# Optimization experiments

Hardware: AMD Instinct MI355X
Metric: run time of the kernel (lower is better)

The kernel has to match this reference:

```python
import jax, jax.numpy as jnp
import numpy as np

B, L, DIM, DFF = 4, 2048, 1024, 4096
EPS = 1e-5

def setup_inputs() -> dict:
    key = jax.random.key(0)
    ks = jax.random.split(key, 10)
    s = 0.02
    return {
        "x": jax.random.normal(ks[0], (B, L, DIM), dtype=jnp.float32),
        "ln_g": jnp.ones((DIM,), jnp.float32),
        "ln_b": jnp.zeros((DIM,), jnp.float32),
        "phazor": jax.random.normal(ks[1], (DIM, 2), dtype=jnp.float32),
        "phazor_init": jax.random.normal(ks[2], (DIM, 2), dtype=jnp.float32),
        "w1": jax.random.normal(ks[3], (DIM, DFF), dtype=jnp.float32) * s,
        "b1": jnp.zeros((DFF,), jnp.float32),
        "w2": jax.random.normal(ks[4], (DFF, DIM), dtype=jnp.float32) * s,
        "b2": jnp.zeros((DIM,), jnp.float32),
        "last_conv_re": jax.random.normal(ks[5], (B, DIM), dtype=jnp.float32),
        "last_conv_im": jax.random.normal(ks[6], (B, DIM), dtype=jnp.float32),
    }

def layer_norm(x, g, b):
    mu = jnp.mean(x, axis=-1, keepdims=True)
    var = jnp.var(x, axis=-1, keepdims=True)
    return (x - mu) * jax.lax.rsqrt(var + EPS) * g + b

def spiral_conv(x, phazor, phazor_init, last_re, last_im):
    # x: [B, L, D] float32
    Lx = x.shape[1]
    p = jax.lax.complex(phazor[:, 0], phazor[:, 1])          # [D]
    p_init = jax.lax.complex(phazor_init[:, 0], phazor_init[:, 1])
    pa = jnp.abs(p)
    p = p / pa * jnp.exp(-pa)                                 # normalized decay phazor
    t = jnp.arange(Lx)
    prog = p[None, :] ** t[:, None]                           # [L, D] p^t
    filt = prog * p_init[None, :]                             # [L, D]
    ffilt = jnp.fft.fft(filt, n=2 * Lx, axis=0)               # [2L, D]
    xf = jnp.fft.fft(x.astype(jnp.complex64), n=2 * Lx, axis=1)  # [B, 2L, D]
    conv = jnp.fft.ifft(ffilt[None] * xf, axis=1)[:, :Lx]     # [B, L, D]
    last = jax.lax.complex(last_re, last_im)                  # [B, D] (detached state)
    conv_with_past = conv + last[:, None, :] * prog[None] * p[None, None, :]
    return conv_with_past.real

def reference(x, ln_g, ln_b, phazor, phazor_init, w1, b1, w2, b2, last_conv_re, last_conv_im):
    x_ = x
    h = layer_norm(x, ln_g, ln_b)
    h = spiral_conv(h, phazor, phazor_init, last_conv_re, last_conv_im)
    x = h + x_
    x_ = x
    h = layer_norm(x, ln_g, ln_b)  # same LayerNorm params reused, as in the source
    h = jax.nn.silu(h @ w1 + b1) @ w2 + b2  # FFN, dropout=0 (eval)
    return h + x_

if __name__ == "__main__":
    out = reference(**setup_inputs())
    print(out.shape, out.dtype)
```

## Files before the change

### kernel.cpp

```cpp
#include <hip/hip_runtime.h>
#include <stdint.h>
#include <stddef.h>

#define DIMC 1024
#define LSEQ 2048
#define BSZ  4
#define DFFC 4096
#define NTOK (BSZ*LSEQ)
#define NCHUNK 32
#define CHUNK 64

typedef __bf16 bf16x8 __attribute__((ext_vector_type(8)));
typedef float  f32x4  __attribute__((ext_vector_type(4)));

__device__ __forceinline__ unsigned short f2bf(float f) {
  unsigned int u = __float_as_uint(f);
  u += 0x7fffu + ((u >> 16) & 1u);
  return (unsigned short)(u >> 16);
}

__device__ __forceinline__ void async16(const void* g, void* l) {
  __builtin_amdgcn_global_load_lds(
      (const __attribute__((address_space(1))) unsigned int*)(uintptr_t)g,
      (__attribute__((address_space(3))) unsigned int*)(uintptr_t)l,
      16, 0, 0);
}

__device__ __forceinline__ void bar() {
  asm volatile("" ::: "memory");
  __builtin_amdgcn_s_barrier();
  asm volatile("" ::: "memory");
}
#define LGKM0 do { asm volatile("s_waitcnt lgkmcnt(0)" ::: "memory"); \
                   __builtin_amdgcn_sched_barrier(0); } while (0)
#define VMCNT(n) asm volatile("s_waitcnt vmcnt(" #n ")" ::: "memory")
template <int N> __device__ __forceinline__ void vmwait() {
  if constexpr (N == 0) VMCNT(0);
  else if constexpr (N == 3) VMCNT(3);
  else if constexpr (N == 4) VMCNT(4);
  else if constexpr (N == 6) VMCNT(6);
  else if constexpr (N == 8) VMCNT(8);
}
#define MFMA_BF16 __builtin_amdgcn_mfma_f32_16x16x32_bf16

__global__ __launch_bounds__(256) void prep(const float* __restrict__ w1,
                                            const float* __restrict__ w2,
                                            unsigned short* __restrict__ w1t,
                                            unsigned short* __restrict__ w2t,
                                            const float* __restrict__ x,
                                            float* __restrict__ mu,
                                            float* __restrict__ rstd,
                                            float* __restrict__ tokstat) {
  __shared__ float tile[32][33];
  __shared__ float sh[8];
  const int blk = blockIdx.x;
  if (blk < 8192) {
    const float* w; unsigned short* wt; int K, N, bi;
    if (blk < 4096) { w = w1; wt = w1t; K = DIMC; N = DFFC; bi = blk; }
    else            { w = w2; wt = w2t; K = DFFC; N = DIMC; bi = blk - 4096; }
    const int nbx = N / 32;
    const int n0 = (bi % nbx) * 32, k0 = (bi / nbx) * 32;
    const int tx = threadIdx.x & 31, ty = threadIdx.x >> 5;
    #pragma unroll
    for (int i = 0; i < 32; i += 8)
      tile[ty + i][tx] = w[(size_t)(k0 + ty + i) * N + n0 + tx];
    __syncthreads();
    #pragma unroll
    for (int i = 0; i < 32; i += 8)
      wt[(size_t)(n0 + ty + i) * K + k0 + tx] = f2bf(tile[tx][ty + i]);
  } else {
    const int token = blk - 8192;
    const float4* xp = (const float4*)(x + (size_t)token * DIMC);
    float4 v = xp[threadIdx.x];
    float s  = v.x + v.y + v.z + v.w;
    float s2 = v.x*v.x + v.y*v.y + v.z*v.z + v.w*v.w;
    #pragma unroll
    for (int o = 32; o; o >>= 1) { s += __shfl_down(s, o); s2 += __shfl_down(s2, o); }
    const int lane = threadIdx.x & 63, w = threadIdx.x >> 6;
    if (lane == 0) { sh[w] = s; sh[4 + w] = s2; }
    __syncthreads();
    if (threadIdx.x == 0) {
      float ts  = sh[0] + sh[1] + sh[2] + sh[3];
      float ts2 = sh[4] + sh[5] + sh[6] + sh[7];
      float m = ts * (1.f / DIMC);
      float var = ts2 * (1.f / DIMC) - m * m;
      mu[token] = m;
      rstd[token] = rsqrtf(var + 1e-5f);
      tokstat[2 * token] = 0.f;
      tokstat[2 * token + 1] = 0.f;
    }
  }
}

__device__ __forceinline__ void get_p(const float* __restrict__ phazor, int d,
                                      float& p_re, float& p_im) {
  float pre = phazor[2 * d], pim = phazor[2 * d + 1];
  float a = sqrtf(pre * pre + pim * pim);
  float sc = expf(-a) / a;
  p_re = pre * sc;
  p_im = pim * sc;
}

__global__ __launch_bounds__(256) void scan_phase1(const float* __restrict__ x,
                                                   const float* __restrict__ mu,
                                                   const float* __restrict__ rstd,
                                                   const float* __restrict__ g,
                                                   const float* __restrict__ bb,
                                                   const float* __restrict__ phazor,
                                                   float* __restrict__ Sre,
                                                   float* __restrict__ Sim) {
  const int d = blockIdx.x * 256 + threadIdx.x;
  const int c = blockIdx.y;
  const int b = blockIdx.z;
  float p_re, p_im; get_p(phazor, d, p_re, p_im);
  const float gd = g[d], bd = bb[d];
  const int t0 = c * CHUNK;
  const float* xp  = x + ((size_t)(b * LSEQ + t0)) * DIMC + d;
  const float* mup = mu + b * LSEQ + t0;
  const float* rp  = rstd + b * LSEQ + t0;
  float r_re = 0.f, r_im = 0.f;
  #pragma unroll
  for (int s8 = 0; s8 < CHUNK; s8 += 8) {
    float xv[8];
    #pragma unroll
    for (int k = 0; k < 8; ++k) xv[k] = xp[(size_t)(s8 + k) * DIMC];
    #pragma unroll
    for (int k = 0; k < 8; ++k) {
      float hv = (xv[k] - mup[s8 + k]) * rp[s8 + k] * gd + bd;
      float nr = p_re * r_re - p_im * r_im + hv;
      float ni = p_re * r_im + p_im * r_re;
      r_re = nr; r_im = ni;
    }
  }
  const int bd_i = b * DIMC + d;
  Sre[c * (BSZ * DIMC) + bd_i] = r_re;
  Sim[c * (BSZ * DIMC) + bd_i] = r_im;
}

__global__ __launch_bounds__(256) void scan_phase3(const float* __restrict__ x,
                                                   const float* __restrict__ mu,
                                                   const float* __restrict__ rstd,
                                                   const float* __restrict__ g,
                                                   const float* __restrict__ bb,
                                                   const float* __restrict__ phazor,
                                                   const float* __restrict__ phazor_init,
                                                   const float* __restrict__ last_re,
                                                   const float* __restrict__ last_im,
                                                   const float* __restrict__ Sre,
                                                   const float* __restrict__ Sim,
                                                   float* __restrict__ x2,
                                                   float* __restrict__ tokstat) {
  __shared__ float shs[CHUNK][4], shs2[CHUNK][4];
  const int d = blockIdx.x * 256 + threadIdx.x;
  const int c = blockIdx.y;
  const int b = blockIdx.z;
  const int lane = threadIdx.x & 63, wv = threadIdx.x >> 6;
  float p_re, p_im; get_p(phazor, d, p_re, p_im);
  const float pi_re = phazor_init[2 * d], pi_im = phazor_init[2 * d + 1];
  const float gd = g[d], bd_ = bb[d];
  const int bd_i = b * DIMC + d;
  float br = p_re, bi = p_im;
  #pragma unroll
  for (int i = 0; i < 6; ++i) { float t = br * br - bi * bi; bi = 2.f * br * bi; br = t; }
  float r_re = 0.f, r_im = 0.f;
  for (int j0 = 0; j0 < c; j0 += 8) {
    float sr[8], si[8];
    const int jn = (c - j0 < 8) ? (c - j0) : 8;
    for (int k = 0; k < jn; ++k) {
      sr[k] = Sre[(j0 + k) * (BSZ * DIMC) + bd_i];
      si[k] = Sim[(j0 + k) * (BSZ * DIMC) + bd_i];
    }
    for (int k = 0; k < jn; ++k) {
      float nr = br * r_re - bi * r_im + sr[k];
      float ni = br * r_im + bi * r_re + si[k];
      r_re = nr; r_im = ni;
    }
  }
  float er = 1.f, ei = 0.f;
  {
    float qr = br, qi = bi;
    int e = c;
    while (e) {
      if (e & 1) { float t = er * qr - ei * qi; ei = er * qi + ei * qr; er = t; }
      float t2 = qr * qr - qi * qi; qi = 2.f * qr * qi; qr = t2;
      e >>= 1;
    }
  }
  const float lre = last_re[bd_i], lim = last_im[bd_i];
  float q_re = lre * er - lim * ei;
  float q_im = lre * ei + lim * er;
  const int t0 = c * CHUNK;
  const float* xp  = x + ((size_t)(b * LSEQ + t0)) * DIMC + d;
  const float* mup = mu + b * LSEQ + t0;
  const float* rp  = rstd + b * LSEQ + t0;
  float* op = x2 + ((size_t)(b * LSEQ + t0)) * DIMC + d;
  #pragma unroll
  for (int s8 = 0; s8 < CHUNK; s8 += 8) {
    float xv[8];
    #pragma unroll
    for (int k = 0; k < 8; ++k) xv[k] = xp[(size_t)(s8 + k) * DIMC];
    #pragma unroll
    for (int k = 0; k < 8; ++k) {
      float hv = (xv[k] - mup[s8 + k]) * rp[s8 + k] * gd + bd_;
      float nr = p_re * r_re - p_im * r_im + hv;
      float ni = p_re * r_im + p_im * r_re;
      r_re = nr; r_im = ni;
      float nq = p_re * q_re - p_im * q_im;
      q_im = p_re * q_im + p_im * q_re;
      q_re = nq;
      float opv = pi_re * r_re - pi_im * r_im + q_re + xv[k];
      op[(size_t)(s8 + k) * DIMC] = opv;
      float a1 = opv, a2 = opv * opv;
      #pragma unroll
      for (int o = 32; o; o >>= 1) { a1 += __shfl_xor(a1, o); a2 += __shfl_xor(a2, o); }
      if (lane == 0) { shs[s8 + k][wv] = a1; shs2[s8 + k][wv] = a2; }
    }
  }
  __syncthreads();
  if (threadIdx.x < CHUNK) {
    const int s = threadIdx.x;
    float s1 = shs[s][0] + shs[s][1] + shs[s][2] + shs[s][3];
    float s2 = shs2[s][0] + shs2[s][1] + shs2[s][2] + shs2[s][3];
    const int tok = b * LSEQ + t0 + s;
    atomicAdd(&tokstat[2 * tok], s1);
    atomicAdd(&tokstat[2 * tok + 1], s2);
  }
}

__global__ __launch_bounds__(256) void ln_apply(const float* __restrict__ x2,
                                                const float* __restrict__ tokstat,
                                                const float* __restrict__ g,
                                                const float* __restrict__ bb,
                                                unsigned short* __restrict__ out) {
  const int token = blockIdx.x;
  const float s1 = tokstat[2 * token], s2 = tokstat[2 * token + 1];
  const float m = s1 * (1.f / DIMC);
  const float var = s2 * (1.f / DIMC) - m * m;
  const float r = rsqrtf(var + 1e-5f);
  float4 v = ((const float4*)(x2 + (size_t)token * DIMC))[threadIdx.x];
  float4 gv = ((const float4*)g)[threadIdx.x];
  float4 bv = ((const float4*)bb)[threadIdx.x];
  ushort4 o;
  o.x = f2bf((v.x - m) * r * gv.x + bv.x);
  o.y = f2bf((v.y - m) * r * gv.y + bv.y);
  o.z = f2bf((v.z - m) * r * gv.z + bv.z);
  o.w = f2bf((v.w - m) * r * gv.w + bv.w);
  ((ushort4*)(out + (size_t)token * DIMC))[threadIdx.x] = o;
}

template<int BN, int EPI>
__global__ __launch_bounds__(512, 2) void gemm8(const unsigned short* __restrict__ A,
                                                const unsigned short* __restrict__ Bt,
                                                const float* __restrict__ bias,
                                                const float* __restrict__ resid,
                                                void* __restrict__ outp,
                                                int M, int N, int K) {
  constexpr int AUS = 256 * 32;
  constexpr int BUS = BN * 32;
  constexpr int BUFUS = 2 * AUS + 2 * BUS;
  constexpr int NI = (BN == 256) ? 4 : 2;
  constexpr int LDSUS = (2 * BUFUS > 65536) ? 2 * BUFUS : 65536;
  __shared__ __align__(16) unsigned short lds[LDSUS];

  const int tid  = threadIdx.x;
  const int lane = tid & 63;
  const int wave = tid >> 6;
  const int wm = (wave & 1) * 128;
  const int wn = (wave >> 1) * (BN / 4);
  const int r15 = lane & 15;
  const int cus = ((lane >> 4) ^ ((r15 >> 1) & 3)) * 8;

  int bid = blockIdx.x;
  const int cpx = gridDim.x >> 3;
  bid = (bid & 7) * cpx + (bid >> 3);
  const int ntn = N / BN;
  const int tm = (bid / ntn) * 256;
  const int tn = (bid % ntn) * BN;
  const int NT = K >> 6;

  f32x4 acc[8][NI];
  #pragma unroll
  for (int i = 0; i < 8; ++i)
    #pragma unroll
    for (int j = 0; j < NI; ++j) acc[i][j] = (f32x4){0.f, 0.f, 0.f, 0.f};

  auto stageA1 = [&](int buf, int kk, int k0, int half) {
    unsigned short* blk = lds + buf * BUFUS + kk * AUS;
    const unsigned short* g = A + (size_t)tm * K + k0 + kk * 32;
    const int s = half * 512 + tid;
    const int row = s >> 2;
    const int cg = (s & 3) ^ ((s >> 3) & 3);
    async16(g + (size_t)row * K + cg * 8, blk + (size_t)s * 8);
  };
  auto stageB1 = [&](int buf, int kk, int k0, int half) {
    unsigned short* blk = lds + buf * BUFUS + 2 * AUS + kk * BUS;
    const unsigned short* g = Bt + (size_t)tn * K + k0 + kk * 32;
    const int s = half * 512 + tid;
    const int row = s >> 2;
    const int cg = (s & 3) ^ ((s >> 3) & 3);
    async16(g + (size_t)row * K + cg * 8, blk + (size_t)s * 8);
  };
  auto stageBb = [&](int buf, int kk, int k0) {
    if constexpr (BN == 256) stageB1(buf, kk, k0, 1);
  };
  auto rdA = [&](int buf, int kk, int mi) -> bf16x8 {
    return *(const bf16x8*)(lds + buf * BUFUS + kk * AUS + (wm + mi * 16 + r15) * 32 + cus);
  };
  auto rdB = [&](int buf, int kk, int ni) -> bf16x8 {
    return *(const bf16x8*)(lds + buf * BUFUS + 2 * AUS + kk * BUS + (wn + ni * 16 + r15) * 32 + cus);
  };

  bf16x8 af[4], bq[NI];
  constexpr int VMS = (BN == 256) ? 8 : 6;
  constexpr int VMP = (BN == 256) ? 4 : 3;

#define PH(buf, kk, mh, BREAD, WAIT, ...)                                       \
  {                                                                             \
    _Pragma("unroll")                                                           \
    for (int q = 0; q < 4; ++q) af[q] = rdA(buf, kk, (mh) * 4 + q);             \
    if (BREAD) {                                                                \
      _Pragma("unroll")                                                         \
      for (int n = 0; n < NI; ++n) bq[n] = rdB(buf, kk, n);                     \
    }                                                                           \
    __VA_ARGS__;                                                                \
    bar(); LGKM0;                                                               \
    __builtin_amdgcn_s_setprio(1);                                              \
    _Pragma("unroll")                                                           \
    for (int q = 0; q < 4; ++q)                                                 \
      _Pragma("unroll")                                                         \
      for (int n = 0; n < NI; ++n)                                              \
        acc[(mh) * 4 + q][n] = MFMA_BF16(af[q], bq[n], acc[(mh) * 4 + q][n], 0, 0, 0); \
    __builtin_amdgcn_s_setprio(0);                                              \
    WAIT;                                                                       \
    bar();                                                                      \
  }

  stageA1(0, 0, 0, 0); stageA1(0, 0, 0, 1); stageB1(0, 0, 0, 0); stageBb(0, 0, 0);
  stageA1(0, 1, 0, 0); stageA1(0, 1, 0, 1); stageB1(0, 1, 0, 0); stageBb(0, 1, 0);
  stageA1(1, 0, 64, 0); stageA1(1, 0, 64, 1); stageB1(1, 0, 64, 0); stageBb(1, 0, 64);
  vmwait<VMS>();
  bar();

  for (int i = 0; i < NT / 2 - 1; ++i) {
    const int kb = (2 * i + 1) * 64, kc = kb + 64, kd = kc + 64;
    PH(0, 0, 0, 1, ((void)0),    stageA1(1, 1, kb, 0); stageA1(1, 1, kb, 1))
    PH(0, 0, 1, 0, vmwait<VMS>(), stageB1(1, 1, kb, 0); stageBb(1, 1, kb))
    PH(0, 1, 0, 1, ((void)0),    stageA1(0, 0, kc, 0); stageA1(0, 0, kc, 1))
    PH(0, 1, 1, 0, vmwait<VMS>(), stageB1(0, 0, kc, 0); stageBb(0, 0, kc))
    PH(1, 0, 0, 1, ((void)0),    stageA1(0, 1, kc, 0); stageA1(0, 1, kc, 1))
    PH(1, 0, 1, 0, vmwait<VMS>(), stageB1(0, 1, kc, 0); stageBb(0, 1, kc))
    PH(1, 1, 0, 1, ((void)0),    stageA1(1, 0, kd, 0); stageA1(1, 0, kd, 1))
    PH(1, 1, 1, 0, vmwait<VMS>(), stageB1(1, 0, kd, 0); stageBb(1, 0, kd))
  }

  {
    const int kb = (NT - 1) * 64;
    PH(0, 0, 0, 1, ((void)0),    stageA1(1, 1, kb, 0); stageA1(1, 1, kb, 1))
    PH(0, 0, 1, 0, vmwait<VMS>(), stageB1(1, 1, kb, 0); stageBb(1, 1, kb))
    PH(0, 1, 0, 1, ((void)0),    ((void)0))
    PH(0, 1, 1, 0, vmwait<VMP>(), ((void)0))
    PH(1, 0, 0, 1, ((void)0),    ((void)0))
    PH(1, 0, 1, 0, vmwait<0>(),  ((void)0))
    PH(1, 1, 0, 1, ((void)0),    ((void)0))
    PH(1, 1, 1, 0, ((void)0),    ((void)0))
  }
#undef PH

  const int rg = (lane >> 4) * 4;
  float bias_r[NI];
  #pragma unroll
  for (int ni = 0; ni < NI; ++ni) bias_r[ni] = bias[tn + wn + ni * 16 + r15];

  bar();
  if constexpr (EPI == 0) {
    unsigned short* C = lds;
    #pragma unroll
    for (int mi = 0; mi < 8; ++mi)
      #pragma unroll
      for (int ni = 0; ni < NI; ++ni) {
        const int c0 = wn + ni * 16 + r15;
        #pragma unroll
        for (int j = 0; j < 4; ++j) {
          const int r = wm + mi * 16 + rg + j;
          const int key = (((r & 3) ^ ((r >> 2) & 3)) << 4);
          float v = acc[mi][ni][j] + bias_r[ni];
          v = v / (1.f + __expf(-v));
          C[r * 256 + (c0 ^ key)] = f2bf(v);
        }
      }
    bar();
    #pragma unroll
    for (int i = 0; i < 16; ++i) {
      const int off = i * 4096 + tid * 8;
      const int r = off >> 8;
      const int pc = off & 255;
      const int key = (((r & 3) ^ ((r >> 2) & 3)) << 4);
      bf16x8 v = *(const bf16x8*)(C + off);
      *(bf16x8*)((unsigned short*)outp + (size_t)(tm + r) * N + tn + (pc ^ key)) = v;
    }
  } else {
    float* C = (float*)lds;
    #pragma unroll
    for (int mi = 0; mi < 8; ++mi)
      #pragma unroll
      for (int ni = 0; ni < NI; ++ni) {
        const int c0 = wn + ni * 16 + r15;
        #pragma unroll
        for (int j = 0; j < 4; ++j) {
          const int r = wm + mi * 16 + rg + j;
          const int key = (((r & 3) ^ ((r >> 2) & 3)) << 4);
          C[r * 128 + (c0 ^ key)] = acc[mi][ni][j] + bias_r[ni];
        }
      }
    bar();
    #pragma unroll
    for (int i = 0; i < 16; ++i) {
      const int off = i * 2048 + tid * 4;
      const int r = off >> 7;
      const int pc = off & 127;
      const int key = (((r & 3) ^ ((r >> 2) & 3)) << 4);
      f32x4 v = *(const f32x4*)(C + off);
      const size_t gaddr = (size_t)(tm + r) * N + tn + (pc ^ key);
      f32x4 rv = *(const f32x4*)(resid + gaddr);
      v += rv;
      *(f32x4*)((float*)outp + gaddr) = v;
    }
  }
}

extern "C" void kernel_launch(void* const* d_in, const int* in_sizes, int n_in,
                              void* d_out, int out_size, void* d_ws, size_t ws_size,
                              hipStream_t stream) {
  const float* x           = (const float*)d_in[0];
  const float* ln_g        = (const float*)d_in[1];
  const float* ln_b        = (const float*)d_in[2];
  const float* phazor      = (const float*)d_in[3];
  const float* phazor_init = (const float*)d_in[4];
  const float* w1          = (const float*)d_in[5];
  const float* b1          = (const float*)d_in[6];
  const float* w2          = (const float*)d_in[7];
  const float* b2          = (const float*)d_in[8];
  const float* last_re     = (const float*)d_in[9];
  const float* last_im     = (const float*)d_in[10];
  float* out = (float*)d_out;
  char* ws = (char*)d_ws;
  const size_t MB = 1ull << 20;

  float* x2  = (float*)(ws);
  float* mu1 = (float*)(ws + 32 * MB);
  float* rs1 = (float*)(ws + 32 * MB + 64 * 1024);
  float* Sre = (float*)(ws + 32 * MB + 256 * 1024);
  float* Sim = (float*)(ws + 32 * MB + 768 * 1024);
  float* tokstat = (float*)(ws + 32 * MB + 1280 * 1024);
  unsigned short* h2  = (unsigned short*)(ws + 35 * MB);
  unsigned short* hid = (unsigned short*)(ws + 51 * MB);
  unsigned short* w1t = (unsigned short*)(ws + 115 * MB);
  unsigned short* w2t = (unsigned short*)(ws + 123 * MB);

  prep<<<16384, 256, 0, stream>>>(w1, w2, w1t, w2t, x, mu1, rs1, tokstat);
  scan_phase1<<<dim3(DIMC / 256, NCHUNK, BSZ), 256, 0, stream>>>(x, mu1, rs1, ln_g, ln_b,
                                                                 phazor, Sre, Sim);
  scan_phase3<<<dim3(DIMC / 256, NCHUNK, BSZ), 256, 0, stream>>>(x, mu1, rs1, ln_g, ln_b, phazor,
                                                                 phazor_init, last_re, last_im,
                                                                 Sre, Sim, x2, tokstat);
  ln_apply<<<NTOK, 256, 0, stream>>>(x2, tokstat, ln_g, ln_b, h2);

  gemm8<256, 0><<<(NTOK / 256) * (DFFC / 256), 512, 0, stream>>>(h2, w1t, b1, nullptr, hid,
                                                                 NTOK, DFFC, DIMC);
  gemm8<128, 1><<<(NTOK / 256) * (DIMC / 128), 512, 0, stream>>>(hid, w2t, b2, x2, out,
                                                                 NTOK, DIMC, DFFC);
}
```

Before: 349.8 us.

## Replace pipelined 256-row GEMM with simple 128x128 single-buffered GEMM

Replaces the hand-scheduled, double-buffered gemm8 (256xBN tiles, 512 threads, phased barriers with priority hints and async prefetch overlap) with a simpler gemm97 that uses 128x128 tiles and 256 threads. It loads each 64-wide K slice into LDS and syncs before computing, with no overlap of loads and MFMA. The residual epilogue is split into two halves to fit the smaller LDS. This gives more, smaller blocks and lower register and LDS use per block, at the cost of less data reuse per tile and no latency hiding in the K loop.

```diff
diff --git a/kernel.cpp b/kernel.cpp
--- a/kernel.cpp
+++ b/kernel.cpp
@@ -26,21 +26,6 @@
       16, 0, 0);
 }
 
-__device__ __forceinline__ void bar() {
-  asm volatile("" ::: "memory");
-  __builtin_amdgcn_s_barrier();
-  asm volatile("" ::: "memory");
-}
-#define LGKM0 do { asm volatile("s_waitcnt lgkmcnt(0)" ::: "memory"); \
-                   __builtin_amdgcn_sched_barrier(0); } while (0)
-#define VMCNT(n) asm volatile("s_waitcnt vmcnt(" #n ")" ::: "memory")
-template <int N> __device__ __forceinline__ void vmwait() {
-  if constexpr (N == 0) VMCNT(0);
-  else if constexpr (N == 3) VMCNT(3);
-  else if constexpr (N == 4) VMCNT(4);
-  else if constexpr (N == 6) VMCNT(6);
-  else if constexpr (N == 8) VMCNT(8);
-}
 #define MFMA_BF16 __builtin_amdgcn_mfma_f32_16x16x32_bf16
 
 __global__ __launch_bounds__(256) void prep(const float* __restrict__ w1,
@@ -248,136 +233,79 @@
   ((ushort4*)(out + (size_t)token * DIMC))[threadIdx.x] = o;
 }
 
-template<int BN, int EPI>
-__global__ __launch_bounds__(512, 2) void gemm8(const unsigned short* __restrict__ A,
-                                                const unsigned short* __restrict__ Bt,
-                                                const float* __restrict__ bias,
-                                                const float* __restrict__ resid,
-                                                void* __restrict__ outp,
-                                                int M, int N, int K) {
-  constexpr int AUS = 256 * 32;
-  constexpr int BUS = BN * 32;
-  constexpr int BUFUS = 2 * AUS + 2 * BUS;
-  constexpr int NI = (BN == 256) ? 4 : 2;
-  constexpr int LDSUS = (2 * BUFUS > 65536) ? 2 * BUFUS : 65536;
-  __shared__ __align__(16) unsigned short lds[LDSUS];
-
+template<int EPI>
+__global__ __launch_bounds__(256) void gemm97(const unsigned short* __restrict__ A,
+                                              const unsigned short* __restrict__ Bt,
+                                              const float* __restrict__ bias,
+                                              const float* __restrict__ resid,
+                                              void* __restrict__ outp,
+                                              int M, int N, int K) {
+  __shared__ __align__(16) unsigned short As[2 * 128 * 32];
+  __shared__ __align__(16) unsigned short Bs[2 * 128 * 32];
   const int tid  = threadIdx.x;
   const int lane = tid & 63;
   const int wave = tid >> 6;
-  const int wm = (wave & 1) * 128;
-  const int wn = (wave >> 1) * (BN / 4);
+  const int wm = (wave & 1) * 64;
+  const int wn = (wave >> 1) * 64;
   const int r15 = lane & 15;
   const int cus = ((lane >> 4) ^ ((r15 >> 1) & 3)) * 8;
 
   int bid = blockIdx.x;
   const int cpx = gridDim.x >> 3;
   bid = (bid & 7) * cpx + (bid >> 3);
-  const int ntn = N / BN;
-  const int tm = (bid / ntn) * 256;
-  const int tn = (bid % ntn) * BN;
-  const int NT = K >> 6;
-
-  f32x4 acc[8][NI];
+  const int ntn = N >> 7;
+  const int tm = (bid / ntn) << 7;
+  const int tn = (bid % ntn) << 7;
+
+  f32x4 acc[4][4];
   #pragma unroll
-  for (int i = 0; i < 8; ++i)
-    #pragma unroll
-    for (int j = 0; j < NI; ++j) acc[i][j] = (f32x4){0.f, 0.f, 0.f, 0.f};
-
-  auto stageA1 = [&](int buf, int kk, int k0, int half) {
-    unsigned short* blk = lds + buf * BUFUS + kk * AUS;
-    const unsigned short* g = A + (size_t)tm * K + k0 + kk * 32;
-    const int s = half * 512 + tid;
-    const int row = s >> 2;
-    const int cg = (s & 3) ^ ((s >> 3) & 3);
-    async16(g + (size_t)row * K + cg * 8, blk + (size_t)s * 8);
-  };
-  auto stageB1 = [&](int buf, int kk, int k0, int half) {
-    unsigned short* blk = lds + buf * BUFUS + 2 * AUS + kk * BUS;
-    const unsigned short* g = Bt + (size_t)tn * K + k0 + kk * 32;
-    const int s = half * 512 + tid;
-    const int row = s >> 2;
-    const int cg = (s & 3) ^ ((s >> 3) & 3);
-    async16(g + (size_t)row * K + cg * 8, blk + (size_t)s * 8);
-  };
-  auto stageBb = [&](int buf, int kk, int k0) {
-    if constexpr (BN == 256) stageB1(buf, kk, k0, 1);
-  };
-  auto rdA = [&](int buf, int kk, int mi) -> bf16x8 {
-    return *(const bf16x8*)(lds + buf * BUFUS + kk * AUS + (wm + mi * 16 + r15) * 32 + cus);
-  };
-  auto rdB = [&](int buf, int kk, int ni) -> bf16x8 {
-    return *(const bf16x8*)(lds + buf * BUFUS + 2 * AUS + kk * BUS + (wn + ni * 16 + r15) * 32 + cus);
-  };
-
-  bf16x8 af[4], bq[NI];
-  constexpr int VMS = (BN == 256) ? 8 : 6;
-  constexpr int VMP = (BN == 256) ? 4 : 3;
-
-#define PH(buf, kk, mh, BREAD, WAIT, ...)                                       \
-  {                                                                             \
-    _Pragma("unroll")                                                           \
-    for (int q = 0; q < 4; ++q) af[q] = rdA(buf, kk, (mh) * 4 + q);             \
-    if (BREAD) {                                                                \
-      _Pragma("unroll")                                                         \
-      for (int n = 0; n < NI; ++n) bq[n] = rdB(buf, kk, n);                     \
-    }                                                                           \
-    __VA_ARGS__;                                                                \
-    bar(); LGKM0;                                                               \
-    __builtin_amdgcn_s_setprio(1);                                              \
-    _Pragma("unroll")                                                           \
-    for (int q = 0; q < 4; ++q)                                                 \
-      _Pragma("unroll")                                                         \
-      for (int n = 0; n < NI; ++n)                                              \
-        acc[(mh) * 4 + q][n] = MFMA_BF16(af[q], bq[n], acc[(mh) * 4 + q][n], 0, 0, 0); \
-    __builtin_amdgcn_s_setprio(0);                                              \
-    WAIT;                                                                       \
-    bar();                                                                      \
-  }
-
-  stageA1(0, 0, 0, 0); stageA1(0, 0, 0, 1); stageB1(0, 0, 0, 0); stageBb(0, 0, 0);
-  stageA1(0, 1, 0, 0); stageA1(0, 1, 0, 1); stageB1(0, 1, 0, 0); stageBb(0, 1, 0);
-  stageA1(1, 0, 64, 0); stageA1(1, 0, 64, 1); stageB1(1, 0, 64, 0); stageBb(1, 0, 64);
-  vmwait<VMS>();
-  bar();
-
-  for (int i = 0; i < NT / 2 - 1; ++i) {
-    const int kb = (2 * i + 1) * 64, kc = kb + 64, kd = kc + 64;
-    PH(0, 0, 0, 1, ((void)0),    stageA1(1, 1, kb, 0); stageA1(1, 1, kb, 1))
-    PH(0, 0, 1, 0, vmwait<VMS>(), stageB1(1, 1, kb, 0); stageBb(1, 1, kb))
-    PH(0, 1, 0, 1, ((void)0),    stageA1(0, 0, kc, 0); stageA1(0, 0, kc, 1))
-    PH(0, 1, 1, 0, vmwait<VMS>(), stageB1(0, 0, kc, 0); stageBb(0, 0, kc))
-    PH(1, 0, 0, 1, ((void)0),    stageA1(0, 1, kc, 0); stageA1(0, 1, kc, 1))
-    PH(1, 0, 1, 0, vmwait<VMS>(), stageB1(0, 1, kc, 0); stageBb(0, 1, kc))
-    PH(1, 1, 0, 1, ((void)0),    stageA1(1, 0, kd, 0); stageA1(1, 0, kd, 1))
-    PH(1, 1, 1, 0, vmwait<VMS>(), stageB1(1, 0, kd, 0); stageBb(1, 0, kd))
-  }
-
-  {
-    const int kb = (NT - 1) * 64;
-    PH(0, 0, 0, 1, ((void)0),    stageA1(1, 1, kb, 0); stageA1(1, 1, kb, 1))
-    PH(0, 0, 1, 0, vmwait<VMS>(), stageB1(1, 1, kb, 0); stageBb(1, 1, kb))
-    PH(0, 1, 0, 1, ((void)0),    ((void)0))
-    PH(0, 1, 1, 0, vmwait<VMP>(), ((void)0))
-    PH(1, 0, 0, 1, ((void)0),    ((void)0))
-    PH(1, 0, 1, 0, vmwait<0>(),  ((void)0))
-    PH(1, 1, 0, 1, ((void)0),    ((void)0))
-    PH(1, 1, 1, 0, ((void)0),    ((void)0))
-  }
-#undef PH
+  for (int i = 0; i < 4; ++i)
+    #pragma unroll
+    for (int j = 0; j < 4; ++j) acc[i][j] = (f32x4){0.f, 0.f, 0.f, 0.f};
+
+  for (int k0 = 0; k0 < K; k0 += 64) {
+    __syncthreads();
+    #pragma unroll
+    for (int s = 0; s < 4; ++s) {
+      const int slot = s * 256 + tid;
+      const int kk = slot >> 9;
+      const int sl = slot & 511;
+      const int row = sl >> 2;
+      const int cg = (sl & 3) ^ ((row >> 1) & 3);
+      const size_t gcol = k0 + kk * 32 + cg * 8;
+      async16(A  + (size_t)(tm + row) * K + gcol, As + kk * 4096 + (size_t)sl * 8);
+      async16(Bt + (size_t)(tn + row) * K + gcol, Bs + kk * 4096 + (size_t)sl * 8);
+    }
+    __syncthreads();
+    #pragma unroll
+    for (int kk = 0; kk < 2; ++kk) {
+      bf16x8 af[4], bv[4];
+      #pragma unroll
+      for (int mi = 0; mi < 4; ++mi)
+        af[mi] = *(const bf16x8*)(As + kk * 4096 + (wm + mi * 16 + r15) * 32 + cus);
+      #pragma unroll
+      for (int ni = 0; ni < 4; ++ni)
+        bv[ni] = *(const bf16x8*)(Bs + kk * 4096 + (wn + ni * 16 + r15) * 32 + cus);
+      #pragma unroll
+      for (int mi = 0; mi < 4; ++mi)
+        #pragma unroll
+        for (int ni = 0; ni < 4; ++ni)
+          acc[mi][ni] = MFMA_BF16(af[mi], bv[ni], acc[mi][ni], 0, 0, 0);
+    }
+  }
 
   const int rg = (lane >> 4) * 4;
-  float bias_r[NI];
+  float bias_r[4];
   #pragma unroll
-  for (int ni = 0; ni < NI; ++ni) bias_r[ni] = bias[tn + wn + ni * 16 + r15];
-
-  bar();
+  for (int ni = 0; ni < 4; ++ni) bias_r[ni] = bias[tn + wn + ni * 16 + r15];
+
+  __syncthreads();
   if constexpr (EPI == 0) {
-    unsigned short* C = lds;
-    #pragma unroll
-    for (int mi = 0; mi < 8; ++mi)
-      #pragma unroll
-      for (int ni = 0; ni < NI; ++ni) {
+    unsigned short* C = As;
+    #pragma unroll
+    for (int mi = 0; mi < 4; ++mi)
+      #pragma unroll
+      for (int ni = 0; ni < 4; ++ni) {
         const int c0 = wn + ni * 16 + r15;
         #pragma unroll
         for (int j = 0; j < 4; ++j) {
@@ -385,45 +313,51 @@
           const int key = (((r & 3) ^ ((r >> 2) & 3)) << 4);
           float v = acc[mi][ni][j] + bias_r[ni];
           v = v / (1.f + __expf(-v));
-          C[r * 256 + (c0 ^ key)] = f2bf(v);
+          C[r * 128 + (c0 ^ key)] = f2bf(v);
         }
       }
-    bar();
-    #pragma unroll
-    for (int i = 0; i < 16; ++i) {
-      const int off = i * 4096 + tid * 8;
-      const int r = off >> 8;
-      const int pc = off & 255;
+    __syncthreads();
+    #pragma unroll
+    for (int i = 0; i < 8; ++i) {
+      const int off = i * 2048 + tid * 8;
+      const int r = off >> 7;
+      const int pc = off & 127;
       const int key = (((r & 3) ^ ((r >> 2) & 3)) << 4);
       bf16x8 v = *(const bf16x8*)(C + off);
       *(bf16x8*)((unsigned short*)outp + (size_t)(tm + r) * N + tn + (pc ^ key)) = v;
     }
   } else {
-    float* C = (float*)lds;
-    #pragma unroll
-    for (int mi = 0; mi < 8; ++mi)
-      #pragma unroll
-      for (int ni = 0; ni < NI; ++ni) {
-        const int c0 = wn + ni * 16 + r15;
+    float* C = (float*)As;
+    #pragma unroll
+    for (int h = 0; h < 2; ++h) {
+      if (wm == h * 64) {
         #pragma unroll
-        for (int j = 0; j < 4; ++j) {
-          const int r = wm + mi * 16 + rg + j;
-          const int key = (((r & 3) ^ ((r >> 2) & 3)) << 4);
-          C[r * 128 + (c0 ^ key)] = acc[mi][ni][j] + bias_r[ni];
-        }
+        for (int mi = 0; mi < 4; ++mi)
+          #pragma unroll
+          for (int ni = 0; ni < 4; ++ni) {
+            const int c0 = wn + ni * 16 + r15;
+            #pragma unroll
+            for (int j = 0; j < 4; ++j) {
+              const int rl = mi * 16 + rg + j;
+              const int key = (((rl & 3) ^ ((rl >> 2) & 3)) << 4);
+              C[rl * 128 + (c0 ^ key)] = acc[mi][ni][j] + bias_r[ni];
+            }
+          }
       }
-    bar();
-    #pragma unroll
-    for (int i = 0; i < 16; ++i) {
-      const int off = i * 2048 + tid * 4;
-      const int r = off >> 7;
-      const int pc = off & 127;
-      const int key = (((r & 3) ^ ((r >> 2) & 3)) << 4);
-      f32x4 v = *(const f32x4*)(C + off);
-      const size_t gaddr = (size_t)(tm + r) * N + tn + (pc ^ key);
-      f32x4 rv = *(const f32x4*)(resid + gaddr);
-      v += rv;
-      *(f32x4*)((float*)outp + gaddr) = v;
+      __syncthreads();
+      #pragma unroll
+      for (int i = 0; i < 8; ++i) {
+        const int off = i * 1024 + tid * 4;
+        const int rl = off >> 7;
+        const int pc = off & 127;
+        const int key = (((rl & 3) ^ ((rl >> 2) & 3)) << 4);
+        f32x4 v = *(const f32x4*)(C + off);
+        const size_t gaddr = (size_t)(tm + h * 64 + rl) * N + tn + (pc ^ key);
+        f32x4 rv = *(const f32x4*)(resid + gaddr);
+        v += rv;
+        *(f32x4*)((float*)outp + gaddr) = v;
+      }
+      __syncthreads();
     }
   }
 }
@@ -465,8 +399,8 @@
                                                                  Sre, Sim, x2, tokstat);
   ln_apply<<<NTOK, 256, 0, stream>>>(x2, tokstat, ln_g, ln_b, h2);
 
-  gemm8<256, 0><<<(NTOK / 256) * (DFFC / 256), 512, 0, stream>>>(h2, w1t, b1, nullptr, hid,
-                                                                 NTOK, DFFC, DIMC);
-  gemm8<128, 1><<<(NTOK / 256) * (DIMC / 128), 512, 0, stream>>>(hid, w2t, b2, x2, out,
-                                                                 NTOK, DIMC, DFFC);
-}
+  gemm97<0><<<(NTOK / 128) * (DFFC / 128), 256, 0, stream>>>(h2, w1t, b1, nullptr, hid,
+                                                             NTOK, DFFC, DIMC);
+  gemm97<1><<<(NTOK / 128) * (DIMC / 128), 256, 0, stream>>>(hid, w2t, b2, x2, out,
+                                                             NTOK, DIMC, DFFC);
+}
```

New measurement: 359.8 us. +2.9%, slower.
